# Kernel optimization log

Measured on AMD Instinct MI355X. Metric: run time of the kernel, lower is better.

The kernel has to match this reference:

```python
import jax, jax.numpy as jnp
import numpy as np

NUM_GROUPS = 32
EPS = 1e-6


def setup_inputs() -> dict:
    key = jax.random.key(0)
    ks = jax.random.split(key, 6)
    n, t, c, h, w = 2, 5, 64, 128, 128
    K = 512  # codebook size
    return {
        "x": jax.random.normal(ks[0], (n, t, c, h, w), dtype=jnp.float32),
        "mb": jax.random.normal(ks[1], (c, K), dtype=jnp.float32),
        "phi_w": jax.random.normal(ks[2], (c, c), dtype=jnp.float32) * (1.0 / np.sqrt(c)),
        "phi_b": jax.random.normal(ks[3], (c,), dtype=jnp.float32) * 0.01,
        "gn_w": jnp.ones((c,), dtype=jnp.float32),
        "gn_b": jnp.zeros((c,), dtype=jnp.float32),
        "wz_w": jax.random.normal(ks[4], (c, c), dtype=jnp.float32) * (1.0 / np.sqrt(c)),
        "wz_b": jax.random.normal(ks[5], (c,), dtype=jnp.float32) * 0.01,
    }


def reference(x, mb, phi_w, phi_b, gn_w, gn_b, wz_w, wz_b):
    n, t, c, h, w = x.shape
    B = n * t
    xf = x.reshape(B, c, h, w)

    # GroupNorm(32 groups, eps=1e-6, affine)
    xg = xf.reshape(B, NUM_GROUPS, c // NUM_GROUPS, h, w)
    mu = jnp.mean(xg, axis=(2, 3, 4), keepdims=True)
    var = jnp.var(xg, axis=(2, 3, 4), keepdims=True)
    xn = ((xg - mu) * jax.lax.rsqrt(var + EPS)).reshape(B, c, h, w)
    xn = xn * gn_w[:, None, None] + gn_b[:, None, None]

    # 1x1 conv phi, flatten spatial -> tokens (B, HW, C)
    phi = jnp.einsum('oc,bchw->bohw', phi_w, xn) + phi_b[:, None, None]
    p = phi.reshape(B, c, h * w).transpose(0, 2, 1)

    # soft-VQ attention against codebook mb (C, K)
    scores = jnp.einsum('bnc,ck->bnk', p, mb) * (c ** -0.5)
    attn = jax.nn.softmax(scores, axis=-1)
    y = jnp.einsum('bnk,ck->bnc', attn, mb)  # (B, HW, C)

    y = y.transpose(0, 2, 1).reshape(B, c, h, w)
    out = jnp.einsum('oc,bchw->bohw', wz_w, y) + wz_b[:, None, None] + xf
    return out.reshape(n, t, c, h, w)
```

## Files before the change

kernel.cpp:

```cpp
#include <hip/hip_runtime.h>


#define HWN 16384
#define CCH 64
#define PSC 0.18033688011112042f

using short8 = __attribute__((ext_vector_type(8))) short;
using f32x4  = __attribute__((ext_vector_type(4))) float;

__device__ __forceinline__ ushort f2bf(float f) {
    union { float f; unsigned int i; } v; v.f = f;
    return (ushort)((v.i + 0x8000u) >> 16);
}
__device__ __forceinline__ unsigned int pk2(float a, float b) {
    union { float f; unsigned int i; } va, vb; va.f = a; vb.f = b;
    return __builtin_amdgcn_perm(vb.i + 0x8000u, va.i + 0x8000u, 0x07060302u);
}

__global__ __launch_bounds__(256) void prep_stats_kernel(
    const float* __restrict__ x, const float* __restrict__ mb,
    const float* __restrict__ phiw, const float* __restrict__ wzw,
    ushort* __restrict__ ws, int nstat)
{
    if (blockIdx.x >= nstat) {
        int i = (blockIdx.x - nstat) * 256 + threadIdx.x;
        int j = i & 7, lane = (i >> 3) & 63, m = lane & 15, q = lane >> 4;
        if (i < 32768) {
            int t = i >> 9, tile = t >> 1, s = t & 1;
            ws[i] = f2bf(mb[(s * 32 + q * 8 + j) * 512 + tile * 16 + m]);
        } else if (i < 65536) {
            int t = (i - 32768) >> 9;
            int mt = t & 3, u2 = t >> 2, s2 = u2 & 1, cc = u2 >> 1;
            ws[i] = f2bf(mb[(mt * 16 + m) * 512 + cc * 64 + s2 * 32 + q * 8 + j]);
        } else if (i < 69632) {
            int t = (i - 65536) >> 9, mt = t >> 1, s = t & 1;
            ws[i] = f2bf(phiw[(mt * 16 + m) * 64 + s * 32 + q * 8 + j]);
        } else {
            int t = (i - 69632) >> 9, mt = t >> 1, s = t & 1;
            ws[i] = f2bf(wzw[(mt * 16 + m) * 64 + s * 32 + q * 8 + j]);
        }
        return;
    }
    float* statf = (float*)(ws + 73728);
    int blk  = blockIdx.x;
    int b    = blk >> 8;
    int g    = (blk >> 3) & 31;
    int part = blk & 7;
    const float4* b4 = (const float4*)(x + (size_t)b * CCH * HWN + (size_t)(g * 2) * HWN) + part * 1024;
    float s = 0.f, s2 = 0.f;
    for (int i = threadIdx.x; i < 1024; i += 256) {
        float4 u = b4[i];
        s  += (u.x + u.y) + (u.z + u.w);
        s2 += (u.x*u.x + u.y*u.y) + (u.z*u.z + u.w*u.w);
    }
    for (int off = 32; off > 0; off >>= 1) {
        s  += __shfl_down(s, off);
        s2 += __shfl_down(s2, off);
    }
    __shared__ float rs[4], rs2[4];
    int wave = threadIdx.x >> 6, lane = threadIdx.x & 63;
    if (lane == 0) { rs[wave] = s; rs2[wave] = s2; }
    __syncthreads();
    if (threadIdx.x == 0) {
        atomicAdd(&statf[b * 32 + g],       rs[0] + rs[1] + rs[2] + rs[3]);
        atomicAdd(&statf[320 + b * 32 + g], rs2[0] + rs2[1] + rs2[2] + rs2[3]);
    }
}

__device__ __forceinline__ void stage_chunk(const ushort* ws, ushort* fg,
                                            int cc, int wv, int lane) {
    const int r = wv >> 1, half = wv & 1;
    const char* g = (const char*)ws + r * 65536 + cc * 8192 + half * 4096 + lane * 16;
    char* l = (char*)fg + r * 8192 + half * 4096;
#pragma unroll
    for (int k = 0; k < 4; ++k)
        __builtin_amdgcn_global_load_lds(
            (const __attribute__((address_space(1))) unsigned int*)(g + k * 1024),
            (__attribute__((address_space(3))) unsigned int*)(l + k * 1024),
            16, 0, 0);
}

__global__ __launch_bounds__(256, 2) void main_mfma(
    const float* __restrict__ x, const ushort* __restrict__ ws,
    const float* __restrict__ phib, const float* __restrict__ gnw,
    const float* __restrict__ gnb, const float* __restrict__ wzb,
    float* __restrict__ out)
{
    const int lane = threadIdx.x & 63, wv = threadIdx.x >> 6;
    const int m = lane & 15, q = lane >> 4;
    const int blk = blockIdx.x;
    const int b   = blk >> 8;
    const int hw0 = ((blk & 255) << 6) + (wv << 4);

    const ushort* phiA = ws + 65536;
    const ushort* wzA  = ws + 69632;
    const float*  statf = (const float*)(ws + 73728);

    __shared__ ushort Fg[2][8192];
    __shared__ ushort Sl[4][2][16 * 72];
    ushort* Ebuf[2] = { &Sl[wv][0][0], &Sl[wv][1][0] };
    ushort* E0 = Ebuf[0];

    const float* xb = x + (size_t)b * CCH * HWN;

    stage_chunk(ws, &Fg[0][0], 0, wv, lane);

    short8 bx[2];
#pragma unroll
    for (int s = 0; s < 2; ++s) {
        const int cbase = s * 32 + q * 8;
        f32x4 sm4 = *(const f32x4*)(statf + b * 32 + (cbase >> 1));
        f32x4 sq4 = *(const f32x4*)(statf + 320 + b * 32 + (cbase >> 1));
        f32x4 mu4, rs4;
#pragma unroll
        for (int r = 0; r < 4; ++r) {
            mu4[r] = sm4[r] * (1.f / 32768.f);
            float var = sq4[r] * (1.f / 32768.f) - mu4[r] * mu4[r];
            rs4[r] = rsqrtf(var + 1e-6f);
        }
        f32x4 gwv0 = *(const f32x4*)(gnw + cbase), gwv1 = *(const f32x4*)(gnw + cbase + 4);
        f32x4 gbv0 = *(const f32x4*)(gnb + cbase), gbv1 = *(const f32x4*)(gnb + cbase + 4);
#pragma unroll
        for (int j = 0; j < 8; ++j) {
            float v  = xb[(size_t)(cbase + j) * HWN + hw0 + m];
            float gw = (j < 4) ? gwv0[j & 3] : gwv1[j & 3];
            float gb = (j < 4) ? gbv0[j & 3] : gbv1[j & 3];
            float xn = (v - mu4[j >> 1]) * rs4[j >> 1] * gw + gb;
            bx[s][j] = (short)f2bf(xn);
        }
    }

#pragma unroll
    for (int mt = 0; mt < 4; ++mt) {
        f32x4 a = (f32x4){0.f,0.f,0.f,0.f};
#pragma unroll
        for (int s = 0; s < 2; ++s) {
            short8 ap = *(const short8*)(phiA + (((mt * 2 + s) * 64 + lane) << 3));
            a = __builtin_amdgcn_mfma_f32_16x16x32_bf16(ap, bx[s], a, 0, 0, 0);
        }
        f32x4 pb = *(const f32x4*)(phib + mt * 16 + q * 4);
        *(uint2*)(E0 + m * 72 + mt * 16 + q * 4) =
            make_uint2(pk2((a[0]+pb[0])*PSC, (a[1]+pb[1])*PSC),
                       pk2((a[2]+pb[2])*PSC, (a[3]+pb[3])*PSC));
    }

    short8 bp[2];
#pragma unroll
    for (int s = 0; s < 2; ++s)
        bp[s] = *(const short8*)(E0 + m * 72 + s * 32 + q * 8);

    __syncthreads();

    f32x4 accY[4];
#pragma unroll
    for (int mt = 0; mt < 4; ++mt) accY[mt] = (f32x4){0.f,0.f,0.f,0.f};
    float lsum = 0.f;

    for (int cc = 0; cc < 8; ++cc) {
        if (cc < 7) stage_chunk(ws, &Fg[(cc + 1) & 1][0], cc + 1, wv, lane);
        const ushort* fA = &Fg[cc & 1][0];
        const ushort* fY = fA + 4096;
        ushort* Eb = Ebuf[cc & 1];
#pragma unroll
        for (int u = 0; u < 4; ++u) {
            short8 am0 = *(const short8*)(fA + (((u * 2 + 0) * 64 + lane) << 3));
            short8 am1 = *(const short8*)(fA + (((u * 2 + 1) * 64 + lane) << 3));
            f32x4 sa = (f32x4){0.f,0.f,0.f,0.f};
            sa = __builtin_amdgcn_mfma_f32_16x16x32_bf16(am0, bp[0], sa, 0, 0, 0);
            sa = __builtin_amdgcn_mfma_f32_16x16x32_bf16(am1, bp[1], sa, 0, 0, 0);
            float e0 = __builtin_exp2f(sa[0]), e1 = __builtin_exp2f(sa[1]);
            float e2 = __builtin_exp2f(sa[2]), e3 = __builtin_exp2f(sa[3]);
            lsum += (e0 + e1) + (e2 + e3);
            *(uint2*)(Eb + m * 72 + u * 16 + q * 4) =
                make_uint2(pk2(e0, e1), pk2(e2, e3));
        }
#pragma unroll
        for (int s2 = 0; s2 < 2; ++s2) {
            short8 be = *(const short8*)(Eb + m * 72 + s2 * 32 + q * 8);
#pragma unroll
            for (int mt = 0; mt < 4; ++mt) {
                short8 ay = *(const short8*)(fY + (((s2 * 4 + mt) * 64 + lane) << 3));
                accY[mt] = __builtin_amdgcn_mfma_f32_16x16x32_bf16(ay, be, accY[mt], 0, 0, 0);
            }
        }
        __syncthreads();
    }

    float l = lsum;
    l += __shfl_xor(l, 16);
    l += __shfl_xor(l, 32);
    const float linv = 1.f / l;

#pragma unroll
    for (int mt = 0; mt < 4; ++mt)
        *(uint2*)(E0 + m * 72 + mt * 16 + q * 4) =
            make_uint2(pk2(accY[mt][0], accY[mt][1]), pk2(accY[mt][2], accY[mt][3]));

    short8 by[2];
#pragma unroll
    for (int s = 0; s < 2; ++s)
        by[s] = *(const short8*)(E0 + m * 72 + s * 32 + q * 8);

    float* ob = out + (size_t)b * CCH * HWN;
#pragma unroll
    for (int mt = 0; mt < 4; ++mt) {
        f32x4 c = (f32x4){0.f,0.f,0.f,0.f};
#pragma unroll
        for (int s = 0; s < 2; ++s) {
            short8 aw = *(const short8*)(wzA + (((mt * 2 + s) * 64 + lane) << 3));
            c = __builtin_amdgcn_mfma_f32_16x16x32_bf16(aw, by[s], c, 0, 0, 0);
        }
        f32x4 wb = *(const f32x4*)(wzb + mt * 16 + q * 4);
#pragma unroll
        for (int r = 0; r < 4; ++r) {
            int o = mt * 16 + q * 4 + r;
            size_t base = (size_t)o * HWN + hw0 + m;
            ob[base] = c[r] * linv + wb[r] + xb[base];
        }
    }
}

extern "C" void kernel_launch(void* const* d_in, const int* in_sizes, int n_in,
                              void* d_out, int out_size, void* d_ws, size_t ws_size,
                              hipStream_t stream) {
    const float* x    = (const float*)d_in[0];
    const float* mb   = (const float*)d_in[1];
    const float* phiw = (const float*)d_in[2];
    const float* phib = (const float*)d_in[3];
    const float* gnw  = (const float*)d_in[4];
    const float* gnb  = (const float*)d_in[5];
    const float* wzw  = (const float*)d_in[6];
    const float* wzb  = (const float*)d_in[7];

    const int B = in_sizes[0] / (CCH * HWN);
    const int nstat = B * 256;

    hipMemsetAsync((char*)d_ws + 36864 * 4, 0, 640 * 4, stream);
    prep_stats_kernel<<<nstat + 288, 256, 0, stream>>>(x, mb, phiw, wzw,
                                                       (ushort*)d_ws, nstat);
    main_mfma<<<B * 256, 256, 0, stream>>>(x, (const ushort*)d_ws,
                                           phib, gnw, gnb, wzb, (float*)d_out);
}
```

Before: 157.7 us.

## Switch main kernel to 32x32x16 MFMA tiles with 32 tokens per wave

Moves all matmuls from 16x16x32 to 32x32x16 bf16 MFMA, so each wave handles 32 tokens instead of 16 and each block handles 128 tokens. The weight and codebook pre-packing is re-laid-out to match the new operand fragment format. Each codebook chunk staged into LDS is now reused across twice as many tokens, and there are fewer MFMA instructions per FLOP. In exchange the grid is halved and register pressure rises from 16-wide accumulators, with occupancy hinted at 3 blocks.

New measurement: 165.2 us. 4.8% more time.

```diff
diff --git a/kernel.cpp b/kernel.cpp
--- a/kernel.cpp
+++ b/kernel.cpp
@@ -4,9 +4,11 @@
 #define HWN 16384
 #define CCH 64
 #define PSC 0.18033688011112042f
+#define ETS 72
 
 using short8 = __attribute__((ext_vector_type(8))) short;
 using f32x4  = __attribute__((ext_vector_type(4))) float;
+using f32x16 = __attribute__((ext_vector_type(16))) float;
 
 __device__ __forceinline__ ushort f2bf(float f) {
     union { float f; unsigned int i; } v; v.f = f;
@@ -24,20 +26,20 @@
 {
     if (blockIdx.x >= nstat) {
         int i = (blockIdx.x - nstat) * 256 + threadIdx.x;
-        int j = i & 7, lane = (i >> 3) & 63, m = lane & 15, q = lane >> 4;
+        int j = i & 7, lane = (i >> 3) & 63;
+        int col = lane & 31, hl = lane >> 5;
         if (i < 32768) {
-            int t = i >> 9, tile = t >> 1, s = t & 1;
-            ws[i] = f2bf(mb[(s * 32 + q * 8 + j) * 512 + tile * 16 + m]);
+            int f = i >> 9, ks = f & 3, u = (f >> 2) & 1, cc = f >> 3;
+            ws[i] = f2bf(mb[(ks * 16 + hl * 8 + j) * 512 + cc * 64 + u * 32 + col]);
         } else if (i < 65536) {
-            int t = (i - 32768) >> 9;
-            int mt = t & 3, u2 = t >> 2, s2 = u2 & 1, cc = u2 >> 1;
-            ws[i] = f2bf(mb[(mt * 16 + m) * 512 + cc * 64 + s2 * 32 + q * 8 + j]);
+            int f = (i - 32768) >> 9, ks = f & 3, t = (f >> 2) & 1, cc = f >> 3;
+            ws[i] = f2bf(mb[(t * 32 + col) * 512 + cc * 64 + ks * 16 + hl * 8 + j]);
         } else if (i < 69632) {
-            int t = (i - 65536) >> 9, mt = t >> 1, s = t & 1;
-            ws[i] = f2bf(phiw[(mt * 16 + m) * 64 + s * 32 + q * 8 + j]);
+            int f = (i - 65536) >> 9, ks = f & 3, t = f >> 2;
+            ws[i] = f2bf(phiw[(t * 32 + col) * 64 + ks * 16 + hl * 8 + j]);
         } else {
-            int t = (i - 69632) >> 9, mt = t >> 1, s = t & 1;
-            ws[i] = f2bf(wzw[(mt * 16 + m) * 64 + s * 32 + q * 8 + j]);
+            int f = (i - 69632) >> 9, ks = f & 3, t = f >> 2;
+            ws[i] = f2bf(wzw[(t * 32 + col) * 64 + ks * 16 + hl * 8 + j]);
         }
         return;
     }
@@ -80,35 +82,35 @@
             16, 0, 0);
 }
 
-__global__ __launch_bounds__(256, 2) void main_mfma(
+__global__ __launch_bounds__(256, 3) void main_mfma(
     const float* __restrict__ x, const ushort* __restrict__ ws,
     const float* __restrict__ phib, const float* __restrict__ gnw,
     const float* __restrict__ gnb, const float* __restrict__ wzb,
     float* __restrict__ out)
 {
     const int lane = threadIdx.x & 63, wv = threadIdx.x >> 6;
-    const int m = lane & 15, q = lane >> 4;
+    const int col = lane & 31, hl = lane >> 5;
     const int blk = blockIdx.x;
-    const int b   = blk >> 8;
-    const int hw0 = ((blk & 255) << 6) + (wv << 4);
+    const int b   = blk >> 7;
+    const int hw0 = ((blk & 127) << 7) + (wv << 5);
+    const int tok = hw0 + col;
 
     const ushort* phiA = ws + 65536;
     const ushort* wzA  = ws + 69632;
     const float*  statf = (const float*)(ws + 73728);
 
     __shared__ ushort Fg[2][8192];
-    __shared__ ushort Sl[4][2][16 * 72];
-    ushort* Ebuf[2] = { &Sl[wv][0][0], &Sl[wv][1][0] };
-    ushort* E0 = Ebuf[0];
+    __shared__ ushort ET[4][32][ETS];
+    ushort* Ew = &ET[wv][col][0];
 
     const float* xb = x + (size_t)b * CCH * HWN;
 
     stage_chunk(ws, &Fg[0][0], 0, wv, lane);
 
-    short8 bx[2];
-#pragma unroll
-    for (int s = 0; s < 2; ++s) {
-        const int cbase = s * 32 + q * 8;
+    short8 bx[4];
+#pragma unroll
+    for (int ks = 0; ks < 4; ++ks) {
+        const int cbase = ks * 16 + hl * 8;
         f32x4 sm4 = *(const f32x4*)(statf + b * 32 + (cbase >> 1));
         f32x4 sq4 = *(const f32x4*)(statf + 320 + b * 32 + (cbase >> 1));
         f32x4 mu4, rs4;
@@ -122,100 +124,120 @@
         f32x4 gbv0 = *(const f32x4*)(gnb + cbase), gbv1 = *(const f32x4*)(gnb + cbase + 4);
 #pragma unroll
         for (int j = 0; j < 8; ++j) {
-            float v  = xb[(size_t)(cbase + j) * HWN + hw0 + m];
+            float v  = xb[(size_t)(cbase + j) * HWN + tok];
             float gw = (j < 4) ? gwv0[j & 3] : gwv1[j & 3];
             float gb = (j < 4) ? gbv0[j & 3] : gbv1[j & 3];
             float xn = (v - mu4[j >> 1]) * rs4[j >> 1] * gw + gb;
-            bx[s][j] = (short)f2bf(xn);
-        }
-    }
-
-#pragma unroll
-    for (int mt = 0; mt < 4; ++mt) {
-        f32x4 a = (f32x4){0.f,0.f,0.f,0.f};
-#pragma unroll
-        for (int s = 0; s < 2; ++s) {
-            short8 ap = *(const short8*)(phiA + (((mt * 2 + s) * 64 + lane) << 3));
-            a = __builtin_amdgcn_mfma_f32_16x16x32_bf16(ap, bx[s], a, 0, 0, 0);
-        }
-        f32x4 pb = *(const f32x4*)(phib + mt * 16 + q * 4);
-        *(uint2*)(E0 + m * 72 + mt * 16 + q * 4) =
-            make_uint2(pk2((a[0]+pb[0])*PSC, (a[1]+pb[1])*PSC),
-                       pk2((a[2]+pb[2])*PSC, (a[3]+pb[3])*PSC));
-    }
-
-    short8 bp[2];
-#pragma unroll
-    for (int s = 0; s < 2; ++s)
-        bp[s] = *(const short8*)(E0 + m * 72 + s * 32 + q * 8);
+            bx[ks][j] = (short)f2bf(xn);
+        }
+    }
+
+#pragma unroll
+    for (int t = 0; t < 2; ++t) {
+        f32x16 P;
+#pragma unroll
+        for (int r = 0; r < 16; ++r) P[r] = 0.f;
+#pragma unroll
+        for (int ks = 0; ks < 4; ++ks) {
+            short8 ap = *(const short8*)(phiA + (((t * 4 + ks) << 9) + (lane << 3)));
+            P = __builtin_amdgcn_mfma_f32_32x32x16_bf16(ap, bx[ks], P, 0, 0, 0);
+        }
+#pragma unroll
+        for (int w = 0; w < 4; ++w) {
+            f32x4 pb = *(const f32x4*)(phib + t * 32 + w * 8 + hl * 4);
+            float v0 = (P[w*4+0] + pb[0]) * PSC, v1 = (P[w*4+1] + pb[1]) * PSC;
+            float v2 = (P[w*4+2] + pb[2]) * PSC, v3 = (P[w*4+3] + pb[3]) * PSC;
+            *(uint2*)(Ew + t * 32 + w * 8 + hl * 4) = make_uint2(pk2(v0, v1), pk2(v2, v3));
+        }
+    }
+    short8 bp[4];
+#pragma unroll
+    for (int ks = 0; ks < 4; ++ks)
+        bp[ks] = *(const short8*)(Ew + ks * 16 + hl * 8);
 
     __syncthreads();
 
-    f32x4 accY[4];
-#pragma unroll
-    for (int mt = 0; mt < 4; ++mt) accY[mt] = (f32x4){0.f,0.f,0.f,0.f};
+    f32x16 accY[2];
+#pragma unroll
+    for (int t = 0; t < 2; ++t)
+#pragma unroll
+        for (int r = 0; r < 16; ++r) accY[t][r] = 0.f;
     float lsum = 0.f;
 
     for (int cc = 0; cc < 8; ++cc) {
         if (cc < 7) stage_chunk(ws, &Fg[(cc + 1) & 1][0], cc + 1, wv, lane);
         const ushort* fA = &Fg[cc & 1][0];
         const ushort* fY = fA + 4096;
-        ushort* Eb = Ebuf[cc & 1];
-#pragma unroll
-        for (int u = 0; u < 4; ++u) {
-            short8 am0 = *(const short8*)(fA + (((u * 2 + 0) * 64 + lane) << 3));
-            short8 am1 = *(const short8*)(fA + (((u * 2 + 1) * 64 + lane) << 3));
-            f32x4 sa = (f32x4){0.f,0.f,0.f,0.f};
-            sa = __builtin_amdgcn_mfma_f32_16x16x32_bf16(am0, bp[0], sa, 0, 0, 0);
-            sa = __builtin_amdgcn_mfma_f32_16x16x32_bf16(am1, bp[1], sa, 0, 0, 0);
-            float e0 = __builtin_exp2f(sa[0]), e1 = __builtin_exp2f(sa[1]);
-            float e2 = __builtin_exp2f(sa[2]), e3 = __builtin_exp2f(sa[3]);
-            lsum += (e0 + e1) + (e2 + e3);
-            *(uint2*)(Eb + m * 72 + u * 16 + q * 4) =
-                make_uint2(pk2(e0, e1), pk2(e2, e3));
-        }
-#pragma unroll
-        for (int s2 = 0; s2 < 2; ++s2) {
-            short8 be = *(const short8*)(Eb + m * 72 + s2 * 32 + q * 8);
-#pragma unroll
-            for (int mt = 0; mt < 4; ++mt) {
-                short8 ay = *(const short8*)(fY + (((s2 * 4 + mt) * 64 + lane) << 3));
-                accY[mt] = __builtin_amdgcn_mfma_f32_16x16x32_bf16(ay, be, accY[mt], 0, 0, 0);
+
+#pragma unroll
+        for (int u = 0; u < 2; ++u) {
+            f32x16 S;
+#pragma unroll
+            for (int r = 0; r < 16; ++r) S[r] = 0.f;
+#pragma unroll
+            for (int ks = 0; ks < 4; ++ks) {
+                short8 am = *(const short8*)(fA + (((u * 4 + ks) << 9) + (lane << 3)));
+                S = __builtin_amdgcn_mfma_f32_32x32x16_bf16(am, bp[ks], S, 0, 0, 0);
             }
-        }
+            float e[16];
+#pragma unroll
+            for (int r = 0; r < 16; ++r) e[r] = __builtin_exp2f(S[r]);
+#pragma unroll
+            for (int r = 0; r < 8; ++r) lsum += e[2*r] + e[2*r+1];
+#pragma unroll
+            for (int w = 0; w < 4; ++w)
+                *(uint2*)(Ew + u * 32 + w * 8 + hl * 4) =
+                    make_uint2(pk2(e[4*w+0], e[4*w+1]), pk2(e[4*w+2], e[4*w+3]));
+        }
+        short8 be[4];
+#pragma unroll
+        for (int ks = 0; ks < 4; ++ks)
+            be[ks] = *(const short8*)(Ew + ks * 16 + hl * 8);
+#pragma unroll
+        for (int t = 0; t < 2; ++t)
+#pragma unroll
+            for (int ks = 0; ks < 4; ++ks) {
+                short8 ay = *(const short8*)(fY + (((t * 4 + ks) << 9) + (lane << 3)));
+                accY[t] = __builtin_amdgcn_mfma_f32_32x32x16_bf16(ay, be[ks], accY[t], 0, 0, 0);
+            }
         __syncthreads();
     }
 
-    float l = lsum;
-    l += __shfl_xor(l, 16);
-    l += __shfl_xor(l, 32);
-    const float linv = 1.f / l;
-
-#pragma unroll
-    for (int mt = 0; mt < 4; ++mt)
-        *(uint2*)(E0 + m * 72 + mt * 16 + q * 4) =
-            make_uint2(pk2(accY[mt][0], accY[mt][1]), pk2(accY[mt][2], accY[mt][3]));
-
-    short8 by[2];
-#pragma unroll
-    for (int s = 0; s < 2; ++s)
-        by[s] = *(const short8*)(E0 + m * 72 + s * 32 + q * 8);
+    lsum += __shfl_xor(lsum, 32);
+    const float linv = 1.f / lsum;
+
+#pragma unroll
+    for (int t = 0; t < 2; ++t)
+#pragma unroll
+        for (int w = 0; w < 4; ++w)
+            *(uint2*)(Ew + t * 32 + w * 8 + hl * 4) =
+                make_uint2(pk2(accY[t][4*w+0], accY[t][4*w+1]),
+                           pk2(accY[t][4*w+2], accY[t][4*w+3]));
+    short8 by[4];
+#pragma unroll
+    for (int ks = 0; ks < 4; ++ks)
+        by[ks] = *(const short8*)(Ew + ks * 16 + hl * 8);
 
     float* ob = out + (size_t)b * CCH * HWN;
 #pragma unroll
-    for (int mt = 0; mt < 4; ++mt) {
-        f32x4 c = (f32x4){0.f,0.f,0.f,0.f};
-#pragma unroll
-        for (int s = 0; s < 2; ++s) {
-            short8 aw = *(const short8*)(wzA + (((mt * 2 + s) * 64 + lane) << 3));
-            c = __builtin_amdgcn_mfma_f32_16x16x32_bf16(aw, by[s], c, 0, 0, 0);
-        }
-        f32x4 wb = *(const f32x4*)(wzb + mt * 16 + q * 4);
-#pragma unroll
-        for (int r = 0; r < 4; ++r) {
-            int o = mt * 16 + q * 4 + r;
-            size_t base = (size_t)o * HWN + hw0 + m;
-            ob[base] = c[r] * linv + wb[r] + xb[base];
+    for (int t = 0; t < 2; ++t) {
+        f32x16 C;
+#pragma unroll
+        for (int r = 0; r < 16; ++r) C[r] = 0.f;
+#pragma unroll
+        for (int ks = 0; ks < 4; ++ks) {
+            short8 aw = *(const short8*)(wzA + (((t * 4 + ks) << 9) + (lane << 3)));
+            C = __builtin_amdgcn_mfma_f32_32x32x16_bf16(aw, by[ks], C, 0, 0, 0);
+        }
+#pragma unroll
+        for (int w = 0; w < 4; ++w) {
+            f32x4 wb = *(const f32x4*)(wzb + t * 32 + w * 8 + hl * 4);
+#pragma unroll
+            for (int r = 0; r < 4; ++r) {
+                int o = t * 32 + w * 8 + hl * 4 + r;
+                size_t base = (size_t)o * HWN + tok;
+                ob[base] = C[w * 4 + r] * linv + wb[r] + xb[base];
+            }
         }
     }
 }
@@ -238,6 +260,6 @@
     hipMemsetAsync((char*)d_ws + 36864 * 4, 0, 640 * 4, stream);
     prep_stats_kernel<<<nstat + 288, 256, 0, stream>>>(x, mb, phiw, wzw,
                                                        (ushort*)d_ws, nstat);
-    main_mfma<<<B * 256, 256, 0, stream>>>(x, (const ushort*)d_ws,
+    main_mfma<<<B * 128, 256, 0, stream>>>(x, (const ushort*)d_ws,
                                            phib, gnw, gnb, wzb, (float*)d_out);
 }
```

## Switch codebook staging to triple-buffered half chunks with vmcnt-based barriers

Applied to the files above, without the earlier changes.

Codebook staging into LDS now uses 32-column half chunks with three rotating buffers instead of 64-column chunks with two. Each sync is a partial s_waitcnt vmcnt plus a raw s_barrier, so the next prefetch stays in flight across the barrier and LDS use shrinks. The per-wave E scratch stride drops from 72 to 40, cutting LDS further, which may help occupancy. The cost is twice as many loop iterations and barriers, plus hand-written waitcnt logic that relies on exact ordering of the async loads.

Result: faster. 151.4 us (-4.0%).

```diff
diff --git a/kernel.cpp b/kernel.cpp
--- a/kernel.cpp
+++ b/kernel.cpp
@@ -4,6 +4,7 @@
 #define HWN 16384
 #define CCH 64
 #define PSC 0.18033688011112042f
+#define ETS 40
 
 using short8 = __attribute__((ext_vector_type(8))) short;
 using f32x4  = __attribute__((ext_vector_type(4))) float;
@@ -68,12 +69,12 @@
 }
 
 __device__ __forceinline__ void stage_chunk(const ushort* ws, ushort* fg,
-                                            int cc, int wv, int lane) {
-    const int r = wv >> 1, half = wv & 1;
-    const char* g = (const char*)ws + r * 65536 + cc * 8192 + half * 4096 + lane * 16;
-    char* l = (char*)fg + r * 8192 + half * 4096;
-#pragma unroll
-    for (int k = 0; k < 4; ++k)
+                                            int hc, int wv, int lane) {
+    const char* g = (const char*)ws + (wv >= 2 ? 65536 : 0) + hc * 4096
+                    + (wv & 1) * 2048 + lane * 16;
+    char* l = (char*)fg + (wv >= 2 ? 4096 : 0) + (wv & 1) * 2048 + lane * 16;
+#pragma unroll
+    for (int k = 0; k < 2; ++k)
         __builtin_amdgcn_global_load_lds(
             (const __attribute__((address_space(1))) unsigned int*)(g + k * 1024),
             (__attribute__((address_space(3))) unsigned int*)(l + k * 1024),
@@ -96,14 +97,14 @@
     const ushort* wzA  = ws + 69632;
     const float*  statf = (const float*)(ws + 73728);
 
-    __shared__ ushort Fg[2][8192];
-    __shared__ ushort Sl[4][2][16 * 72];
+    __shared__ ushort Fg[3][4096];
+    __shared__ ushort Sl[4][2][16 * ETS];
     ushort* Ebuf[2] = { &Sl[wv][0][0], &Sl[wv][1][0] };
-    ushort* E0 = Ebuf[0];
 
     const float* xb = x + (size_t)b * CCH * HWN;
 
     stage_chunk(ws, &Fg[0][0], 0, wv, lane);
+    stage_chunk(ws, &Fg[1][0], 1, wv, lane);
 
     short8 bx[2];
 #pragma unroll
@@ -139,7 +140,7 @@
             a = __builtin_amdgcn_mfma_f32_16x16x32_bf16(ap, bx[s], a, 0, 0, 0);
         }
         f32x4 pb = *(const f32x4*)(phib + mt * 16 + q * 4);
-        *(uint2*)(E0 + m * 72 + mt * 16 + q * 4) =
+        *(uint2*)(Ebuf[mt >> 1] + m * ETS + (mt & 1) * 16 + q * 4) =
             make_uint2(pk2((a[0]+pb[0])*PSC, (a[1]+pb[1])*PSC),
                        pk2((a[2]+pb[2])*PSC, (a[3]+pb[3])*PSC));
     }
@@ -147,22 +148,27 @@
     short8 bp[2];
 #pragma unroll
     for (int s = 0; s < 2; ++s)
-        bp[s] = *(const short8*)(E0 + m * 72 + s * 32 + q * 8);
-
-    __syncthreads();
+        bp[s] = *(const short8*)(Ebuf[s] + m * ETS + q * 8);
+
+    asm volatile("s_waitcnt vmcnt(2)" ::: "memory");
+    __builtin_amdgcn_s_barrier();
 
     f32x4 accY[4];
 #pragma unroll
     for (int mt = 0; mt < 4; ++mt) accY[mt] = (f32x4){0.f,0.f,0.f,0.f};
     float lsum = 0.f;
 
-    for (int cc = 0; cc < 8; ++cc) {
-        if (cc < 7) stage_chunk(ws, &Fg[(cc + 1) & 1][0], cc + 1, wv, lane);
-        const ushort* fA = &Fg[cc & 1][0];
-        const ushort* fY = fA + 4096;
-        ushort* Eb = Ebuf[cc & 1];
-#pragma unroll
-        for (int u = 0; u < 4; ++u) {
+    ushort* f0 = &Fg[0][0];
+    ushort* f1 = &Fg[1][0];
+    ushort* f2 = &Fg[2][0];
+
+    for (int hc = 0; hc < 16; ++hc) {
+        if (hc < 14) stage_chunk(ws, f2, hc + 2, wv, lane);
+        const ushort* fA = f0;
+        const ushort* fY = f0 + 2048;
+        ushort* Eb = Ebuf[hc & 1];
+#pragma unroll
+        for (int u = 0; u < 2; ++u) {
             short8 am0 = *(const short8*)(fA + (((u * 2 + 0) * 64 + lane) << 3));
             short8 am1 = *(const short8*)(fA + (((u * 2 + 1) * 64 + lane) << 3));
             f32x4 sa = (f32x4){0.f,0.f,0.f,0.f};
@@ -171,19 +177,25 @@
             float e0 = __builtin_exp2f(sa[0]), e1 = __builtin_exp2f(sa[1]);
             float e2 = __builtin_exp2f(sa[2]), e3 = __builtin_exp2f(sa[3]);
             lsum += (e0 + e1) + (e2 + e3);
-            *(uint2*)(Eb + m * 72 + u * 16 + q * 4) =
+            *(uint2*)(Eb + m * ETS + u * 16 + q * 4) =
                 make_uint2(pk2(e0, e1), pk2(e2, e3));
         }
-#pragma unroll
-        for (int s2 = 0; s2 < 2; ++s2) {
-            short8 be = *(const short8*)(Eb + m * 72 + s2 * 32 + q * 8);
+        {
+            short8 be = *(const short8*)(Eb + m * ETS + q * 8);
 #pragma unroll
             for (int mt = 0; mt < 4; ++mt) {
-                short8 ay = *(const short8*)(fY + (((s2 * 4 + mt) * 64 + lane) << 3));
+                short8 ay = *(const short8*)(fY + (((mt * 64 + lane)) << 3));
                 accY[mt] = __builtin_amdgcn_mfma_f32_16x16x32_bf16(ay, be, accY[mt], 0, 0, 0);
             }
         }
-        __syncthreads();
+        if (hc < 14) {
+            asm volatile("s_waitcnt vmcnt(2)" ::: "memory");
+            __builtin_amdgcn_s_barrier();
+        } else if (hc == 14) {
+            asm volatile("s_waitcnt vmcnt(0)" ::: "memory");
+            __builtin_amdgcn_s_barrier();
+        }
+        ushort* t = f0; f0 = f1; f1 = f2; f2 = t;
     }
 
     float l = lsum;
@@ -193,13 +205,13 @@
 
 #pragma unroll
     for (int mt = 0; mt < 4; ++mt)
-        *(uint2*)(E0 + m * 72 + mt * 16 + q * 4) =
+        *(uint2*)(Ebuf[mt >> 1] + m * ETS + (mt & 1) * 16 + q * 4) =
             make_uint2(pk2(accY[mt][0], accY[mt][1]), pk2(accY[mt][2], accY[mt][3]));
 
     short8 by[2];
 #pragma unroll
     for (int s = 0; s < 2; ++s)
-        by[s] = *(const short8*)(E0 + m * 72 + s * 32 + q * 8);
+        by[s] = *(const short8*)(Ebuf[s] + m * ETS + q * 8);
 
     float* ob = out + (size_t)b * CCH * HWN;
 #pragma unroll
```
